# Kernel optimization log

Measured on AMD Instinct MI355X. Metric: run time of the kernel, lower is better.

Reference implementation:

```python
import jax, jax.numpy as jnp
import numpy as np

S = 7  # YOLOv1 grid size


def _iou(a, b):
    # a, b: [..., 4] corner boxes (x1, y1, x2, y2); eps matches global get_iou (1e-7)
    xl = jnp.maximum(a[..., 0], b[..., 0])
    yt = jnp.maximum(a[..., 1], b[..., 1])
    xr = jnp.minimum(a[..., 2], b[..., 2])
    yb = jnp.minimum(a[..., 3], b[..., 3])
    ix = jnp.maximum(xr - xl, 0.0)
    iy = jnp.maximum(yb - yt, 0.0)
    inter = ix * iy
    aa = jnp.abs((a[..., 2] - a[..., 0]) * (a[..., 3] - a[..., 1]))
    ba = jnp.abs((b[..., 2] - b[..., 0]) * (b[..., 3] - b[..., 1]))
    return inter / (aa + ba - inter + 1e-7)


def setup_inputs() -> dict:
    key = jax.random.key(0)
    k1, k2, k3 = jax.random.split(key, 3)
    N, C = 8192, 30  # 5 * num_bboxes(2) + num_classes(20)
    modely = jax.random.normal(k1, (N, S, S, C), dtype=jnp.float32)
    targety = jax.random.uniform(k2, (N, S, S, C), dtype=jnp.float32)
    # keep target wh strictly positive so sqrt(target_wh) is well-behaved
    targety = targety.at[..., 2:4].set(targety[..., 2:4] * 0.9 + 0.05)
    obj = (jax.random.uniform(k3, (N, S, S)) < 0.3).astype(jnp.float32)
    targety = targety.at[..., 4].set(obj)
    targety = targety.at[..., 9].set(obj)
    return {"modely": modely, "targety": targety}


def reference(modely, targety):
    p, t = modely, targety
    # lt_norm: meshgrid 'xy' -> lt[i, j] = (j, i) / S
    cell_x, cell_y = np.meshgrid(np.arange(S), np.arange(S))
    lt = jnp.asarray(np.dstack([cell_x, cell_y]).astype(np.float32)) / S  # [7,7,2]

    coord = (t[..., 4] > 0).astype(p.dtype)   # [N,7,7]
    noobj = (t[..., 4] == 0).astype(p.dtype)  # [N,7,7]

    # predicted box 1: corners from center-offset/size parametrization
    p_xy1 = lt + p[..., 0:2] / S - p[..., 2:4] / 2
    b1 = jnp.concatenate([p_xy1, p[..., 2:4] + p_xy1], axis=-1)
    # predicted box 2: faithfully replicates the source (uses p[...,5:7]/2, not p[...,7:9]/2)
    p_xy2 = lt + p[..., 5:7] * (1.0 / S - 0.5)
    b2 = jnp.concatenate([p_xy2, p[..., 7:9] + p_xy2], axis=-1)
    # target box
    t_xy = lt + t[..., 0:2] / S - t[..., 2:4] / 2
    tb = jnp.concatenate([t_xy, t[..., 2:4] + t_xy], axis=-1)

    iou1 = _iou(b1, tb)  # [N,7,7]
    iou2 = _iou(b2, tb)
    sel = (iou1 >= iou2)[..., None]
    # best box (raw network values, like modely[coord_mask][:, :10][high_bbox])
    box = jnp.where(sel, p[..., 0:5], p[..., 5:10])  # [N,7,7,5]

    xy_se = jnp.sum(coord * jnp.sum((box[..., 0:2] - t[..., 0:2]) ** 2, axis=-1))
    wh_p = jnp.sign(box[..., 2:4]) * jnp.sqrt(jnp.abs(box[..., 2:4]))
    wh_se = jnp.sum(coord * jnp.sum((wh_p - jnp.sqrt(t[..., 2:4])) ** 2, axis=-1))
    obj_se = jnp.sum(coord * (jnp.maximum(iou1, iou2) - box[..., 4]) ** 2)
    noobj_se = jnp.sum(noobj * ((p[..., 4] - t[..., 4]) ** 2 + (p[..., 9] - t[..., 9]) ** 2))
    label_se = jnp.sum(coord * jnp.sum((p[..., 10:] - t[..., 10:]) ** 2, axis=-1))

    loss = 5.0 * (xy_se + wh_se) + obj_se + 0.5 * noobj_se + label_se
    return loss / t.shape[0]
```

## Files before the change

### kernel.cpp

```cpp
#include <hip/hip_runtime.h>


#define NCH 30
#define CELLS_PER_SAMPLE 49
#define CPB 256
#define F4_PER_ARR 1920
#define F4_TOTAL  3840
#define NLOAD 15

__device__ __forceinline__ float iou_f(float a0, float a1, float a2, float a3,
                                       float b0, float b1, float b2, float b3) {
    float xl = fmaxf(a0, b0);
    float yt = fmaxf(a1, b1);
    float xr = fminf(a2, b2);
    float yb = fminf(a3, b3);
    float ix = fmaxf(xr - xl, 0.0f);
    float iy = fmaxf(yb - yt, 0.0f);
    float inter = ix * iy;
    float aa = fabsf((a2 - a0) * (a3 - a1));
    float ba = fabsf((b2 - b0) * (b3 - b1));
    return inter / (aa + ba - inter + 1e-7f);
}

__device__ __forceinline__ float cell_loss_f(const float* __restrict__ pv,
                                             const float* __restrict__ tv,
                                             int cell) {
    int rem = cell % CELLS_PER_SAMPLE;
    int ci = rem / 7;
    int cj = rem % 7;

    float ltx = (float)cj / 7.0f;
    float lty = (float)ci / 7.0f;

    float coord = (tv[4] > 0.0f) ? 1.0f : 0.0f;
    float noobj = (tv[4] == 0.0f) ? 1.0f : 0.0f;

    float b1x1 = ltx + pv[0] / 7.0f - pv[2] * 0.5f;
    float b1y1 = lty + pv[1] / 7.0f - pv[3] * 0.5f;
    float b1x2 = pv[2] + b1x1;
    float b1y2 = pv[3] + b1y1;

    const float C2 = (float)(1.0 / 7.0 - 0.5);
    float b2x1 = ltx + pv[5] * C2;
    float b2y1 = lty + pv[6] * C2;
    float b2x2 = pv[7] + b2x1;
    float b2y2 = pv[8] + b2y1;

    float tbx1 = ltx + tv[0] / 7.0f - tv[2] * 0.5f;
    float tby1 = lty + tv[1] / 7.0f - tv[3] * 0.5f;
    float tbx2 = tv[2] + tbx1;
    float tby2 = tv[3] + tby1;

    float iou1 = iou_f(b1x1, b1y1, b1x2, b1y2, tbx1, tby1, tbx2, tby2);
    float iou2 = iou_f(b2x1, b2y1, b2x2, b2y2, tbx1, tby1, tbx2, tby2);

    bool sel = (iou1 >= iou2);
    float bx = sel ? pv[0] : pv[5];
    float by = sel ? pv[1] : pv[6];
    float bw = sel ? pv[2] : pv[7];
    float bh = sel ? pv[3] : pv[8];
    float bc = sel ? pv[4] : pv[9];

    float dx = bx - tv[0];
    float dy = by - tv[1];
    float xy_se = dx * dx + dy * dy;

    float sw = (bw > 0.0f) ? 1.0f : ((bw < 0.0f) ? -1.0f : 0.0f);
    float sh = (bh > 0.0f) ? 1.0f : ((bh < 0.0f) ? -1.0f : 0.0f);
    float dw = sw * sqrtf(fabsf(bw)) - sqrtf(tv[2]);
    float dh = sh * sqrtf(fabsf(bh)) - sqrtf(tv[3]);
    float wh_se = dw * dw + dh * dh;

    float mio = fmaxf(iou1, iou2);
    float dob = mio - bc;
    float obj_se = dob * dob;

    float d4 = pv[4] - tv[4];
    float d9 = pv[9] - tv[9];
    float noobj_se = d4 * d4 + d9 * d9;

    float lab = 0.0f;
    #pragma unroll
    for (int k = 10; k < NCH; ++k) {
        float d = pv[k] - tv[k];
        lab += d * d;
    }

    return coord * (5.0f * (xy_se + wh_se) + obj_se + lab)
         + 0.5f * noobj * noobj_se;
}

__global__ __launch_bounds__(256, 2) void yolo_loss_kernel(
    const float4* __restrict__ p4, const float4* __restrict__ t4,
    float* __restrict__ out, float inv_n)
{
    __shared__ float4 lds[F4_TOTAL];
    __shared__ float wave_sums[4];

    const int tid = threadIdx.x;
    const float4* __restrict__ pb = p4 + (size_t)blockIdx.x * F4_PER_ARR;
    const float4* __restrict__ tb = t4 + (size_t)blockIdx.x * F4_PER_ARR;

    float4 r[NLOAD];
    #pragma unroll
    for (int i = 0; i < NLOAD; ++i) {
        int idx = tid + i * CPB;
        const float4* src = (idx < F4_PER_ARR) ? (pb + idx)
                                               : (tb + (idx - F4_PER_ARR));
        r[i] = *src;
    }
    #pragma unroll
    for (int i = 0; i < NLOAD; ++i)
        lds[tid + i * CPB] = r[i];
    __syncthreads();

    const float* pvp = (const float*)lds + tid * NCH;
    const float* tvp = (const float*)lds + F4_PER_ARR * 4 + tid * NCH;

    float pv[NCH], tv[NCH];
    #pragma unroll
    for (int k = 0; k < NCH / 2; ++k) {
        float2 a = ((const float2*)pvp)[k];
        float2 b = ((const float2*)tvp)[k];
        pv[2 * k] = a.x; pv[2 * k + 1] = a.y;
        tv[2 * k] = b.x; tv[2 * k + 1] = b.y;
    }

    float acc = cell_loss_f(pv, tv, blockIdx.x * CPB + tid) * inv_n;

    #pragma unroll
    for (int off = 32; off > 0; off >>= 1)
        acc += __shfl_down(acc, off, 64);

    int lane = tid & 63;
    int wid  = tid >> 6;
    if (lane == 0) wave_sums[wid] = acc;
    __syncthreads();
    if (tid == 0) {
        float s = wave_sums[0] + wave_sums[1] + wave_sums[2] + wave_sums[3];
        atomicAdd(out, s);
    }
}

extern "C" void kernel_launch(void* const* d_in, const int* in_sizes, int n_in,
                              void* d_out, int out_size, void* d_ws, size_t ws_size,
                              hipStream_t stream) {
    const float4* p = (const float4*)d_in[0];
    const float4* t = (const float4*)d_in[1];
    float* out = (float*)d_out;

    int ncells = in_sizes[0] / NCH;
    int nsamples = ncells / CELLS_PER_SAMPLE;
    int blocks = ncells / CPB;

    hipMemsetAsync(out, 0, sizeof(float) * (size_t)out_size, stream);

    yolo_loss_kernel<<<blocks, 256, 0, stream>>>(
        p, t, out, 1.0f / (float)nsamples);
}
```

Baseline: 117.3 us.

## Use persistent blocks with register prefetch and two-stage deterministic reduction

Switches from one block per 256-cell chunk to 512 persistent blocks that loop over chunks. Each block prefetches the next chunk into registers while it computes the current chunk from LDS. The global atomicAdd and memset are replaced by per-block partials written to the workspace, which a second single-block kernel then sums. The aim is to overlap memory loads with compute and to drop the atomic contention and memset launch. In exchange it adds an extra kernel launch, extra barriers per iteration, and fewer blocks in flight to hide latency.

```diff
diff --git a/kernel.cpp b/kernel.cpp
--- a/kernel.cpp
+++ b/kernel.cpp
@@ -7,6 +7,7 @@
 #define F4_PER_ARR 1920
 #define F4_TOTAL  3840
 #define NLOAD 15
+#define NBLK 512
 
 __device__ __forceinline__ float iou_f(float a0, float a1, float a2, float a3,
                                        float b0, float b1, float b2, float b3) {
@@ -90,18 +91,12 @@
          + 0.5f * noobj * noobj_se;
 }
 
-__global__ __launch_bounds__(256, 2) void yolo_loss_kernel(
-    const float4* __restrict__ p4, const float4* __restrict__ t4,
-    float* __restrict__ out, float inv_n)
-{
-    __shared__ float4 lds[F4_TOTAL];
-    __shared__ float wave_sums[4];
-
-    const int tid = threadIdx.x;
-    const float4* __restrict__ pb = p4 + (size_t)blockIdx.x * F4_PER_ARR;
-    const float4* __restrict__ tb = t4 + (size_t)blockIdx.x * F4_PER_ARR;
-
-    float4 r[NLOAD];
+__device__ __forceinline__ void load_regs(float4* r,
+                                          const float4* __restrict__ p4,
+                                          const float4* __restrict__ t4,
+                                          int chunk, int tid) {
+    const float4* pb = p4 + (size_t)chunk * F4_PER_ARR;
+    const float4* tb = t4 + (size_t)chunk * F4_PER_ARR;
     #pragma unroll
     for (int i = 0; i < NLOAD; ++i) {
         int idx = tid + i * CPB;
@@ -109,24 +104,59 @@
                                                : (tb + (idx - F4_PER_ARR));
         r[i] = *src;
     }
-    #pragma unroll
-    for (int i = 0; i < NLOAD; ++i)
-        lds[tid + i * CPB] = r[i];
-    __syncthreads();
-
-    const float* pvp = (const float*)lds + tid * NCH;
-    const float* tvp = (const float*)lds + F4_PER_ARR * 4 + tid * NCH;
-
-    float pv[NCH], tv[NCH];
-    #pragma unroll
-    for (int k = 0; k < NCH / 2; ++k) {
-        float2 a = ((const float2*)pvp)[k];
-        float2 b = ((const float2*)tvp)[k];
-        pv[2 * k] = a.x; pv[2 * k + 1] = a.y;
-        tv[2 * k] = b.x; tv[2 * k + 1] = b.y;
-    }
-
-    float acc = cell_loss_f(pv, tv, blockIdx.x * CPB + tid) * inv_n;
+}
+
+__global__ __launch_bounds__(256, 2) void yolo_loss_kernel(
+    const float4* __restrict__ p4, const float4* __restrict__ t4,
+    float* __restrict__ partials, int nchunks, float inv_n)
+{
+    __shared__ float4 lds[F4_TOTAL];
+    __shared__ float wave_sums[4];
+
+    const int tid = threadIdx.x;
+    float acc = 0.0f;
+    float4 r[NLOAD];
+
+    int c = blockIdx.x;
+    if (c < nchunks) {
+        load_regs(r, p4, t4, c, tid);
+        #pragma unroll
+        for (int i = 0; i < NLOAD; ++i)
+            lds[tid + i * CPB] = r[i];
+        __syncthreads();
+    }
+
+    while (c < nchunks) {
+        int cn = c + NBLK;
+        bool have_next = (cn < nchunks);
+        if (have_next)
+            load_regs(r, p4, t4, cn, tid);
+
+        {
+            const float* pvp = (const float*)lds + tid * NCH;
+            const float* tvp = (const float*)lds + F4_PER_ARR * 4 + tid * NCH;
+            float pv[NCH], tv[NCH];
+            #pragma unroll
+            for (int k = 0; k < NCH / 2; ++k) {
+                float2 a = ((const float2*)pvp)[k];
+                float2 b = ((const float2*)tvp)[k];
+                pv[2 * k] = a.x; pv[2 * k + 1] = a.y;
+                tv[2 * k] = b.x; tv[2 * k + 1] = b.y;
+            }
+            acc += cell_loss_f(pv, tv, c * CPB + tid);
+        }
+
+        if (have_next) {
+            __syncthreads();
+            #pragma unroll
+            for (int i = 0; i < NLOAD; ++i)
+                lds[tid + i * CPB] = r[i];
+            __syncthreads();
+        }
+        c = cn;
+    }
+
+    acc *= inv_n;
 
     #pragma unroll
     for (int off = 32; off > 0; off >>= 1)
@@ -136,9 +166,29 @@
     int wid  = tid >> 6;
     if (lane == 0) wave_sums[wid] = acc;
     __syncthreads();
+    if (tid == 0)
+        partials[blockIdx.x] = wave_sums[0] + wave_sums[1]
+                             + wave_sums[2] + wave_sums[3];
+}
+
+__global__ __launch_bounds__(512) void reduce_kernel(
+    const float* __restrict__ partials, float* __restrict__ out)
+{
+    __shared__ float wave_sums[8];
+    int tid = threadIdx.x;
+    float v = partials[tid];
+    #pragma unroll
+    for (int off = 32; off > 0; off >>= 1)
+        v += __shfl_down(v, off, 64);
+    int lane = tid & 63;
+    int wid  = tid >> 6;
+    if (lane == 0) wave_sums[wid] = v;
+    __syncthreads();
     if (tid == 0) {
-        float s = wave_sums[0] + wave_sums[1] + wave_sums[2] + wave_sums[3];
-        atomicAdd(out, s);
+        float s = 0.0f;
+        #pragma unroll
+        for (int i = 0; i < 8; ++i) s += wave_sums[i];
+        out[0] = s;
     }
 }
 
@@ -148,13 +198,13 @@
     const float4* p = (const float4*)d_in[0];
     const float4* t = (const float4*)d_in[1];
     float* out = (float*)d_out;
+    float* partials = (float*)d_ws;
 
     int ncells = in_sizes[0] / NCH;
     int nsamples = ncells / CELLS_PER_SAMPLE;
-    int blocks = ncells / CPB;
-
-    hipMemsetAsync(out, 0, sizeof(float) * (size_t)out_size, stream);
-
-    yolo_loss_kernel<<<blocks, 256, 0, stream>>>(
-        p, t, out, 1.0f / (float)nsamples);
-}
+    int nchunks = ncells / CPB;
+
+    yolo_loss_kernel<<<NBLK, 256, 0, stream>>>(
+        p, t, partials, nchunks, 1.0f / (float)nsamples);
+    reduce_kernel<<<1, 512, 0, stream>>>(partials, out);
+}
```

New measurement: 136.2 us. +16.1%, slower.

## Use persistent single-wave blocks with grid-stride tiles and two-pass reduction

Applied to the files above, without the earlier changes.

Replaces the one-tile-per-256-thread-block launch with a fixed grid of 2560 single-wavefront blocks. Each block loops over 64-cell tiles, staging them through LDS and accumulating a per-lane sum. Per-block partials go to workspace and a second single-block kernel sums them, which drops the memset and global atomics. In exchange it adds a second launch and a loop-carried barrier, and each tile load has less memory-level parallelism per block.

```diff
diff --git a/kernel.cpp b/kernel.cpp
--- a/kernel.cpp
+++ b/kernel.cpp
@@ -3,10 +3,11 @@
 
 #define NCH 30
 #define CELLS_PER_SAMPLE 49
-#define CPB 256
-#define F4_PER_ARR 1920
-#define F4_TOTAL  3840
+#define TILE_CELLS 64
+#define F4_PER_ARR 480
+#define F4_TOTAL   960
 #define NLOAD 15
+#define NBLK 2560
 
 __device__ __forceinline__ float iou_f(float a0, float a1, float a2, float a3,
                                        float b0, float b1, float b2, float b3) {
@@ -90,56 +91,78 @@
          + 0.5f * noobj * noobj_se;
 }
 
-__global__ __launch_bounds__(256, 2) void yolo_loss_kernel(
+__global__ __launch_bounds__(64) void yolo_loss_kernel(
     const float4* __restrict__ p4, const float4* __restrict__ t4,
-    float* __restrict__ out, float inv_n)
+    float* __restrict__ partials, int ntiles, float inv_n)
 {
     __shared__ float4 lds[F4_TOTAL];
-    __shared__ float wave_sums[4];
+    const int lane = threadIdx.x;
 
-    const int tid = threadIdx.x;
-    const float4* __restrict__ pb = p4 + (size_t)blockIdx.x * F4_PER_ARR;
-    const float4* __restrict__ tb = t4 + (size_t)blockIdx.x * F4_PER_ARR;
+    float acc = 0.0f;
 
-    float4 r[NLOAD];
-    #pragma unroll
-    for (int i = 0; i < NLOAD; ++i) {
-        int idx = tid + i * CPB;
-        const float4* src = (idx < F4_PER_ARR) ? (pb + idx)
-                                               : (tb + (idx - F4_PER_ARR));
-        r[i] = *src;
-    }
-    #pragma unroll
-    for (int i = 0; i < NLOAD; ++i)
-        lds[tid + i * CPB] = r[i];
-    __syncthreads();
+    for (int tile = blockIdx.x; tile < ntiles; tile += NBLK) {
+        const float4* pb = p4 + (size_t)tile * F4_PER_ARR;
+        const float4* tb = t4 + (size_t)tile * F4_PER_ARR;
 
-    const float* pvp = (const float*)lds + tid * NCH;
-    const float* tvp = (const float*)lds + F4_PER_ARR * 4 + tid * NCH;
+        float4 r[NLOAD];
+        #pragma unroll
+        for (int i = 0; i < NLOAD; ++i) {
+            int idx = lane + i * 64;
+            const float4* src = (idx < F4_PER_ARR) ? (pb + idx)
+                                                   : (tb + (idx - F4_PER_ARR));
+            r[i] = *src;
+        }
+        #pragma unroll
+        for (int i = 0; i < NLOAD; ++i)
+            lds[lane + i * 64] = r[i];
+        __syncthreads();
 
-    float pv[NCH], tv[NCH];
-    #pragma unroll
-    for (int k = 0; k < NCH / 2; ++k) {
-        float2 a = ((const float2*)pvp)[k];
-        float2 b = ((const float2*)tvp)[k];
-        pv[2 * k] = a.x; pv[2 * k + 1] = a.y;
-        tv[2 * k] = b.x; tv[2 * k + 1] = b.y;
+        {
+            const float* pvp = (const float*)lds + lane * NCH;
+            const float* tvp = (const float*)lds + F4_PER_ARR * 4 + lane * NCH;
+            float pv[NCH], tv[NCH];
+            #pragma unroll
+            for (int k = 0; k < NCH / 2; ++k) {
+                float2 a = ((const float2*)pvp)[k];
+                float2 b = ((const float2*)tvp)[k];
+                pv[2 * k] = a.x; pv[2 * k + 1] = a.y;
+                tv[2 * k] = b.x; tv[2 * k + 1] = b.y;
+            }
+            acc += cell_loss_f(pv, tv, tile * TILE_CELLS + lane);
+        }
+        __syncthreads();
     }
 
-    float acc = cell_loss_f(pv, tv, blockIdx.x * CPB + tid) * inv_n;
+    acc *= inv_n;
 
     #pragma unroll
     for (int off = 32; off > 0; off >>= 1)
         acc += __shfl_down(acc, off, 64);
 
+    if (lane == 0) partials[blockIdx.x] = acc;
+}
+
+__global__ __launch_bounds__(256) void reduce_kernel(
+    const float* __restrict__ partials, float* __restrict__ out)
+{
+    __shared__ float wave_sums[4];
+    const int tid = threadIdx.x;
+
+    float v = 0.0f;
+    #pragma unroll
+    for (int j = 0; j < NBLK / 256; ++j)
+        v += partials[tid + j * 256];
+
+    #pragma unroll
+    for (int off = 32; off > 0; off >>= 1)
+        v += __shfl_down(v, off, 64);
+
     int lane = tid & 63;
     int wid  = tid >> 6;
-    if (lane == 0) wave_sums[wid] = acc;
+    if (lane == 0) wave_sums[wid] = v;
     __syncthreads();
-    if (tid == 0) {
-        float s = wave_sums[0] + wave_sums[1] + wave_sums[2] + wave_sums[3];
-        atomicAdd(out, s);
-    }
+    if (tid == 0)
+        out[0] = wave_sums[0] + wave_sums[1] + wave_sums[2] + wave_sums[3];
 }
 
 extern "C" void kernel_launch(void* const* d_in, const int* in_sizes, int n_in,
@@ -148,13 +171,13 @@
     const float4* p = (const float4*)d_in[0];
     const float4* t = (const float4*)d_in[1];
     float* out = (float*)d_out;
+    float* partials = (float*)d_ws;
 
     int ncells = in_sizes[0] / NCH;
     int nsamples = ncells / CELLS_PER_SAMPLE;
-    int blocks = ncells / CPB;
+    int ntiles = ncells / TILE_CELLS;
 
-    hipMemsetAsync(out, 0, sizeof(float) * (size_t)out_size, stream);
-
-    yolo_loss_kernel<<<blocks, 256, 0, stream>>>(
-        p, t, out, 1.0f / (float)nsamples);
+    yolo_loss_kernel<<<NBLK, 64, 0, stream>>>(
+        p, t, partials, ntiles, 1.0f / (float)nsamples);
+    reduce_kernel<<<1, 256, 0, stream>>>(partials, out);
 }
```

Result: faster. 112.9 us (-3.8%).
